# Kernel tuning notes

Measured on AMD Instinct MI355X. Metric: run time of the kernel, lower is better.

The kernel has to match this reference:

```python
import jax, jax.numpy as jnp
import numpy as np

D_IN, H, V = 512, 1024, 32000
S, B, T = 64, 128, 48
MARGIN = 0.1


def setup_inputs() -> dict:
    key = jax.random.key(0)
    ks = jax.random.split(key, 16)
    sc = 0.05
    f = lambda k, shp: jax.random.normal(k, shp, jnp.float32) * sc
    emb_W = f(ks[0], (V, D_IN)).at[0].set(0.0)  # padding_idx=0 row is zero
    return dict(
        ctx=jax.random.normal(ks[1], (S, B, H), jnp.float32),
        ctx_mask=jnp.ones((S, B), jnp.float32),
        y=jax.random.randint(ks[2], (T, B), 0, V),
        emb_W=emb_W,
        W_init=f(ks[3], (H, H)), b_init=jnp.zeros((H,), jnp.float32),
        W_ih0=f(ks[4], (3 * H, D_IN)), W_hh0=f(ks[5], (3 * H, H)),
        b_ih0=jnp.zeros((3 * H,), jnp.float32), b_hh0=jnp.zeros((3 * H,), jnp.float32),
        W_c2c=f(ks[6], (H, H)), W_h2c=f(ks[7], (H, H)), v_att=f(ks[8], (H,)),
        W_ih1=f(ks[9], (3 * H, H)), W_hh1=f(ks[10], (3 * H, H)),
        b_ih1=jnp.zeros((3 * H,), jnp.float32), b_hh1=jnp.zeros((3 * H,), jnp.float32),
        W_h2o=f(ks[11], (D_IN, H)), b_h2o=jnp.zeros((D_IN,), jnp.float32),
        W_out=f(ks[12], (V, D_IN)),
    )


def _gru(x, h, Wih, Whh, bih, bhh):
    # torch.nn.GRUCell math
    gi = x @ Wih.T + bih
    gh = h @ Whh.T + bhh
    ir, iz, inn = jnp.split(gi, 3, axis=-1)
    hr, hz, hn = jnp.split(gh, 3, axis=-1)
    r = jax.nn.sigmoid(ir + hr)
    z = jax.nn.sigmoid(iz + hz)
    n = jnp.tanh(inn + r * hn)
    return (1.0 - z) * n + z * h


def reference(ctx, ctx_mask, y, emb_W, W_init, b_init, W_ih0, W_hh0, b_ih0, b_hh0,
              W_c2c, W_h2c, v_att, W_ih1, W_hh1, b_ih1, b_hh1, W_h2o, b_h2o, W_out):
    # dec_init='mean_ctx': tanh(FF(masked mean over source))
    mean_ctx = ctx.sum(0) / ctx_mask.sum(0)[:, None]            # (B,H)
    h = jnp.tanh(mean_ctx @ W_init.T + b_init)                  # h0 (B,H)

    ctx_p = jnp.einsum('sbc,dc->sbd', ctx, W_c2c)               # ctx2ctx, hoisted out of loop
    neg = jnp.where(ctx_mask > 0, 0.0, -1e9)                    # (S,B) additive mask
    W_out_n = W_out / jnp.linalg.norm(W_out, axis=-1, keepdims=True)

    emb_in = emb_W[y[:-1]]                                      # (T-1,B,D_IN)
    targets = y[1:]                                             # (T-1,B)

    def step(h, inp):
        e, tgt = inp
        h1 = _gru(e, h, W_ih0, W_hh0, b_ih0, b_hh0)             # dec0
        # MLP attention: v^T tanh(ctx2ctx(ctx) + hid2ctx(h1))
        scores = jnp.tanh(ctx_p + (h1 @ W_h2c.T)[None]) @ v_att + neg   # (S,B)
        alpha = jax.nn.softmax(scores, axis=0)
        z_t = jnp.einsum('sb,sbc->bc', alpha, ctx)              # context (B,H)
        h2 = _gru(z_t, h1, W_ih1, W_hh1, b_ih1, b_hh1)          # dec1
        logit = jnp.tanh(h2 @ W_h2o.T + b_h2o)                  # hid2out
        logit = logit / jnp.linalg.norm(logit, axis=-1, keepdims=True)
        log_p = logit @ W_out_n.T                               # (B,V) cosine sims
        # max-margin loss, contrastive_type='max', ignore pad (tgt==0)
        s_true = jnp.take_along_axis(log_p, tgt[:, None], axis=1)
        viol = jnp.maximum(MARGIN - s_true + log_p, 0.0)
        viol = viol * (1.0 - jax.nn.one_hot(tgt, V, dtype=log_p.dtype))
        l = jnp.sum(jnp.where(tgt != 0, viol.max(-1), 0.0))
        return h2, l

    _, losses = jax.lax.scan(step, h, (emb_in, targets))
    return losses.sum()
```

## Files before the change

### kernel.cpp

```cpp
#include <hip/hip_runtime.h>
#include <math.h>

#define H    1024
#define H3   3072
#define DIN  512
#define VSZ  32000
#define SS   64
#define BB   128
#define TP   47
#define NROWS (TP*BB)
#define VCHUNKS 250
#define FMARGIN 0.1f
#define NBLK 256
#define HS   65536
#define CTXPL_S 62

typedef unsigned short u16;
typedef unsigned int u32;
typedef unsigned long long u64;
typedef __bf16 bf16_t;
typedef bf16_t bf16x8 __attribute__((ext_vector_type(8)));
typedef float f32x4 __attribute__((ext_vector_type(4)));
typedef u16 u16x4 __attribute__((ext_vector_type(4)));
typedef u16 u16x8 __attribute__((ext_vector_type(8)));

#define MFMA __builtin_amdgcn_mfma_f32_16x16x32_bf16

__device__ inline u16 f2bf(float f){
    unsigned b = __float_as_uint(f);
    return (u16)((b + 0x7FFFu + ((b >> 16) & 1u)) >> 16);
}
__device__ inline float bf2f(u16 u){ return __uint_as_float(((unsigned)u) << 16); }
__device__ inline float sigm(float x){ return 1.f/(1.f + expf(-x)); }

__device__ inline void stoval(float* p, float v){ *p = v; }
__device__ inline void stoval(u16* p, float v){ *p = f2bf(v); }

__device__ inline void cstore(u32* p, u32 v){ __hip_atomic_store(p, v, __ATOMIC_RELAXED, __HIP_MEMORY_SCOPE_AGENT); }
__device__ inline void cstoref(float* p, float v){ __hip_atomic_store(p, v, __ATOMIC_RELAXED, __HIP_MEMORY_SCOPE_AGENT); }
__device__ inline void cstore64(u64* p, u64 v){ __hip_atomic_store(p, v, __ATOMIC_RELAXED, __HIP_MEMORY_SCOPE_AGENT); }
__device__ inline float cloadf(const float* p){ return __hip_atomic_load(p, __ATOMIC_RELAXED, __HIP_MEMORY_SCOPE_AGENT); }

__device__ inline void gbar(u32* bar, u32* mygen, int tid, int bid){
    __syncthreads();
    if (tid == 0){
        u32 tgt = ++(*mygen);
        __builtin_amdgcn_s_waitcnt(0);
        u32* cnt = bar + 64 + (bid >> 3)*32;
        u32 old = __hip_atomic_fetch_add(cnt, 1u, __ATOMIC_RELAXED, __HIP_MEMORY_SCOPE_AGENT);
        if (old == 7u){
            __hip_atomic_store(cnt, 0u, __ATOMIC_RELAXED, __HIP_MEMORY_SCOPE_AGENT);
            u32 old2 = __hip_atomic_fetch_add(&bar[1], 1u, __ATOMIC_RELEASE, __HIP_MEMORY_SCOPE_AGENT);
            if (old2 == 31u){
                __hip_atomic_store(&bar[1], 0u, __ATOMIC_RELAXED, __HIP_MEMORY_SCOPE_AGENT);
                #pragma unroll
                for (int x = 0; x < 8; x++)
                    __hip_atomic_store(&bar[1536 + x*32], tgt, __ATOMIC_RELEASE, __HIP_MEMORY_SCOPE_AGENT);
            }
        }
        u32* rel = &bar[1536 + (bid & 7)*32];
        while (__hip_atomic_load(rel, __ATOMIC_RELAXED, __HIP_MEMORY_SCOPE_AGENT) < tgt)
            __builtin_amdgcn_s_sleep(2);
    }
    __syncthreads();
    asm volatile("" ::: "memory");
}


__global__ __launch_bounds__(128) void k_mask_sum(const float* __restrict__ mask, float* __restrict__ msum){
    int b = threadIdx.x;
    if (b < BB){ float s = 0.f; for (int i = 0; i < SS; i++) s += mask[i*BB + b]; msum[b] = s; }
}

__global__ __launch_bounds__(256) void k_mean_ctx(const float* __restrict__ ctx, const float* __restrict__ msum,
                                                  float* __restrict__ mean){
    int idx = blockIdx.x*256 + threadIdx.x;
    if (idx < BB*H){
        float s = 0.f;
        for (int i = 0; i < SS; i++) s += ctx[(size_t)i*BB*H + idx];
        mean[idx] = s / msum[idx / H];
    }
}

__global__ __launch_bounds__(256) void k_f32bf(const float* __restrict__ in, u16* __restrict__ out, int n4){
    int i = blockIdx.x*256 + threadIdx.x;
    if (i >= n4) return;
    float4 v = ((const float4*)in)[i];
    u16x4 o = { f2bf(v.x), f2bf(v.y), f2bf(v.z), f2bf(v.w) };
    ((u16x4*)out)[i] = o;
}

__global__ __launch_bounds__(256) void k_pack_h0(const float* __restrict__ h0, u32* __restrict__ hsHI,
                                                 u32* __restrict__ hsLO){
    int i = blockIdx.x*256 + threadIdx.x;
    float v0 = h0[i*2], v1 = h0[i*2 + 1];
    u16 a = f2bf(v0), b = f2bf(v1);
    hsHI[i] = (u32)a | ((u32)b << 16);
    hsLO[i] = (u32)f2bf(v0 - bf2f(a)) | ((u32)f2bf(v1 - bf2f(b)) << 16);
}

__global__ __launch_bounds__(256) void k_f2bf_frag(const float* __restrict__ in, u16* __restrict__ out,
                                                   int RK8, int K8){
    int t = blockIdx.x*256 + threadIdx.x;
    if (t >= RK8) return;
    int r = t / K8, k8 = t - r*K8;
    const float* p = in + (size_t)r*K8*8 + k8*8;
    float4 a = *(const float4*)p;
    float4 b = *(const float4*)(p + 4);
    size_t dst = ((size_t)(r >> 4)*(K8 >> 2) + (k8 >> 2))*512 + (size_t)((r & 15) + (k8 & 3)*16)*8;
    u16x8 o;
    o[0]=f2bf(a.x); o[1]=f2bf(a.y); o[2]=f2bf(a.z); o[3]=f2bf(a.w);
    o[4]=f2bf(b.x); o[5]=f2bf(b.y); o[6]=f2bf(b.z); o[7]=f2bf(b.w);
    *(u16x8*)(out + dst) = o;
}

// ... 69 lines not shown
        #pragma unroll
        for (int j = 0; j < 4; j++){
            float v = acc[i][j];
            if (bias) v += bias[bn + tc + j];
            if (ACT == 1) v = tanhf(v);
            C[(size_t)(bm + tr + i)*N + bn + tc + j] = v;
        }
    }
}

template<int AFRAG, int ACT, typename OutT>
__global__ __launch_bounds__(256) void k_gemmf(const u16* __restrict__ A, const u16* __restrict__ B,
                                               const float* __restrict__ bias, OutT* __restrict__ C,
                                               int M, int N, int K){
    int tid = threadIdx.x, lane = tid & 63, w = tid >> 6;
    int wm = w >> 1, wn = w & 1;
    int row0 = blockIdx.y*128 + wm*64, col0 = blockIdx.x*128 + wn*64;
    int r16 = lane & 15, kg8 = (lane >> 4)*8, rg = (lane >> 4)*4;
    int K32 = K >> 5;
    f32x4 acc[4][4] = {};
    for (int k0 = 0; k0 < K32; k0++){
        bf16x8 af[4], bfv[4];
        #pragma unroll
        for (int i = 0; i < 4; i++){
            if (AFRAG) af[i] = *(const bf16x8*)(A + (((size_t)((row0 >> 4) + i)*K32 + k0) << 9) + lane*8);
            else       af[i] = *(const bf16x8*)(A + (size_t)(row0 + i*16 + r16)*K + k0*32 + kg8);
        }
        #pragma unroll
        for (int j = 0; j < 4; j++)
            bfv[j] = *(const bf16x8*)(B + (((size_t)((col0 >> 4) + j)*K32 + k0) << 9) + lane*8);
        #pragma unroll
        for (int i = 0; i < 4; i++)
            #pragma unroll
            for (int j = 0; j < 4; j++)
                acc[i][j] = MFMA(af[i], bfv[j], acc[i][j], 0, 0, 0);
    }
    #pragma unroll
    for (int i = 0; i < 4; i++){
        #pragma unroll
        for (int j = 0; j < 4; j++){
            #pragma unroll
            for (int r = 0; r < 4; r++){
                int row = row0 + i*16 + rg + r;
                int col = col0 + j*16 + r16;
                float v = acc[i][j][r];
                if (bias) v += bias[col];
                if (ACT) v = tanhf(v);
                stoval(C + (size_t)row*N + col, v);
            }
        }
    }
}

struct RJ {
    const u16 *gi0, *Whh0, *Wh2c, *Wih1, *Whh1, *ctxp;
    const float *bhh0, *bih1, *bhh1, *vatt, *mask, *ctxf;
    u32 *hsHI, *hsLO, *h1HI, *h1LO, *ztHI, *ztLO;
    float *prF;
    float *ghF;
    float *spar;
    u32 *flg;
    u16 *h2all;
    u32 *bar;
};

__global__ __launch_bounds__(512) void k_recur9(RJ a){
    __shared__ u16 wlds[49152];
    __shared__ u16 ctxpL[CTXPL_S*512];
    __shared__ float sal[SS];
    const int tid = threadIdx.x, lane = tid & 63, wv = tid >> 6;
    const int bid = blockIdx.x;
    const int r16 = lane & 15, rg = (lane >> 4)*4, kq4 = (lane >> 4)*4;
    const int ab = (bid & 7)*16 + ((bid >> 3) >> 1);
    const int ahalf = (bid >> 3) & 1;
    u32 mygen = 0;

    {
        auto cp32k = [&](const u16* gsrc, int tile, int base){
            const u32* s = (const u32*)(gsrc + (size_t)tile*16384);
            u32* d = (u32*)(wlds + base);
            #pragma unroll
            for (int i = 0; i < 16; i++) d[tid + i*512] = s[tid + i*512];
        };
        if (bid < 64){
            cp32k(a.Whh0, bid, 0); cp32k(a.Whh0, 64+bid, 16384); cp32k(a.Whh0, 128+bid, 32768);
        } else if (bid < 128){
            int jt = bid - 64;
            cp32k(a.Wih1, jt, 0); cp32k(a.Wih1, 64+jt, 16384); cp32k(a.Wih1, 128+jt, 32768);
        } else if (bid < 192){
            int wt = bid - 128;
            cp32k(a.Whh1, 3*wt, 0); cp32k(a.Whh1, 3*wt+1, 16384); cp32k(a.Whh1, 3*wt+2, 32768);
        } else {
            cp32k(a.Wh2c, bid-192, 0);
        }
        for (int i = tid; i < CTXPL_S*512/8; i += 512){
            int s = (i*8) >> 9, h = (i*8) & 511;
            *(u16x8*)(ctxpL + i*8) = *(const u16x8*)(a.ctxp + ((size_t)(s*BB + ab))*H + ahalf*512 + h);
        }
    }
    float vv[8];
    {
        float4 v0 = *(const float4*)(a.vatt + ahalf*512 + lane*8);
        float4 v1 = *(const float4*)(a.vatt + ahalf*512 + lane*8 + 4);
        vv[0]=v0.x; vv[1]=v0.y; vv[2]=v0.z; vv[3]=v0.w;
        vv[4]=v1.x; vv[5]=v1.y; vv[6]=v1.z; vv[7]=v1.w;
    }
    __syncthreads();

    for (int t = 0; t < TP; t++){
        float* prT = a.prF + (size_t)t*BB*H;
        float* spT = a.spar + (size_t)t*256*SS;

        if (bid < 64){
            const u32* AbH = a.hsHI + (size_t)t*HS + (size_t)(wv*16 + r16)*512 + kq4;
            const u32* AbL = a.hsLO + (size_t)t*HS + (size_t)(wv*16 + r16)*512 + kq4;
            f32x4 ac0 = {}, ac1 = {}, ac2 = {};
            for (int k0 = 0; k0 < 32; k0++){
                bf16x8 ah = *(const bf16x8*)(AbH + k0*16);
                bf16x8 al = *(const bf16x8*)(AbL + k0*16);
                bf16x8 b0 = *(const bf16x8*)(wlds + (k0*64 + lane)*8);
                bf16x8 b1 = *(const bf16x8*)(wlds + 16384 + (k0*64 + lane)*8);
                bf16x8 b2 = *(const bf16x8*)(wlds + 32768 + (k0*64 + lane)*8);
                ac0 = MFMA(ah, b0, ac0, 0, 0, 0); ac0 = MFMA(al, b0, ac0, 0, 0, 0);
                ac1 = MFMA(ah, b1, ac1, 0, 0, 0); ac1 = MFMA(al, b1, ac1, 0, 0, 0);
                ac2 = MFMA(ah, b2, ac2, 0, 0, 0); ac2 = MFMA(al, b2, ac2, 0, 0, 0);
            }
            const u16* gi = a.gi0 + (size_t)t*BB*H3;
            const u32* hsH = a.hsHI + (size_t)t*HS;
            const u32* hsL = a.hsLO + (size_t)t*HS;
            int sh = (r16 & 1)*16;
            #pragma unroll
            for (int r = 0; r < 4; r++){
                int b = wv*16 + rg + r, j = bid*16 + r16;
                float gr = bf2f(gi[(size_t)b*H3 + j]);
                float gz = bf2f(gi[(size_t)b*H3 + H + j]);
                float gn = bf2f(gi[(size_t)b*H3 + 2*H + j]);
                float hr = ac0[r] + a.bhh0[j];
                float hz = ac1[r] + a.bhh0[H + j];
                float hn = ac2[r] + a.bhh0[2*H + j];
                u32 uh = hsH[(size_t)b*512 + (j >> 1)];
                u32 ul = hsL[(size_t)b*512 + (j >> 1)];
                float hp = bf2f((u16)(uh >> sh)) + bf2f((u16)(ul >> sh));
                float rr = sigm(gr + hr), zz = sigm(gz + hz);
                float nn = tanhf(gn + rr*hn);
                float hv = (1.f - zz)*nn + zz*hp;
                u16 hib = f2bf(hv);
                u16 lob = f2bf(hv - bf2f(hib));
                u32 hip = (u32)__shfl_xor((int)(u32)hib, 1);
                u32 lop = (u32)__shfl_xor((int)(u32)lob, 1);
                if (!(r16 & 1)){
                    cstore(a.h1HI + (size_t)t*HS + (size_t)b*512 + (j >> 1), (u32)hib | (hip << 16));
                    cstore(a.h1LO + (size_t)t*HS + (size_t)b*512 + (j >> 1), (u32)lob | (lop << 16));
                }
            }
        }
        gbar(a.bar, &mygen, tid, bid);

        if (bid >= 128){
            const u32* AbH = a.h1HI + (size_t)t*HS + (size_t)(wv*16 + r16)*512 + kq4;
            const u32* AbL = a.h1LO + (size_t)t*HS + (size_t)(wv*16 + r16)*512 + kq4;
            if (bid < 192){
                int wt = bid - 128;
                f32x4 ac0 = {}, ac1 = {}, ac2 = {};
                for (int k0 = 0; k0 < 32; k0++){
                    bf16x8 ah = *(const bf16x8*)(AbH + k0*16);
                    bf16x8 al = *(const bf16x8*)(AbL + k0*16);
                    bf16x8 b0 = *(const bf16x8*)(wlds + (k0*64 + lane)*8);
                    bf16x8 b1 = *(const bf16x8*)(wlds + 16384 + (k0*64 + lane)*8);
                    bf16x8 b2 = *(const bf16x8*)(wlds + 32768 + (k0*64 + lane)*8);
                    ac0 = MFMA(ah, b0, ac0, 0, 0, 0); ac0 = MFMA(al, b0, ac0, 0, 0, 0);
                    ac1 = MFMA(ah, b1, ac1, 0, 0, 0); ac1 = MFMA(al, b1, ac1, 0, 0, 0);
                    ac2 = MFMA(ah, b2, ac2, 0, 0, 0); ac2 = MFMA(al, b2, ac2, 0, 0, 0);
                }
                #pragma unroll
                for (int r = 0; r < 4; r++){
                    int b = wv*16 + rg + r;
                    int c0 = wt*48 + r16;
                    float p0 = __shfl_xor(ac0[r], 1);
                    float p1 = __shfl_xor(ac1[r], 1);
                    float p2 = __shfl_xor(ac2[r], 1);
                    if (!(r16 & 1)){
                        cstore64((u64*)(a.ghF + (size_t)b*H3 + c0),
                                 (u64)__float_as_uint(ac0[r]) | ((u64)__float_as_uint(p0) << 32));
                        cstore64((u64*)(a.ghF + (size_t)b*H3 + c0 + 16),
                                 (u64)__float_as_uint(ac1[r]) | ((u64)__float_as_uint(p1) << 32));
                        cstore64((u64*)(a.ghF + (size_t)b*H3 + c0 + 32),
                                 (u64)__float_as_uint(ac2[r]) | ((u64)__float_as_uint(p2) << 32));
                    }
                }
            } else {
                f32x4 ac = {};
                for (int k0 = 0; k0 < 32; k0++){
                    bf16x8 ah = *(const bf16x8*)(AbH + k0*16);
                    bf16x8 al = *(const bf16x8*)(AbL + k0*16);
                    bf16x8 bv = *(const bf16x8*)(wlds + (k0*64 + lane)*8);
                    ac = MFMA(ah, bv, ac, 0, 0, 0); ac = MFMA(al, bv, ac, 0, 0, 0);
                }
                #pragma unroll
                for (int r = 0; r < 4; r++){
                    int b = wv*16 + rg + r;
                    int c0 = (bid - 192)*16 + r16;
                    float p0 = __shfl_xor(ac[r], 1);
                    if (!(r16 & 1))
                        cstore64((u64*)(prT + (size_t)b*H + c0),
                                 (u64)__float_as_uint(ac[r]) | ((u64)__float_as_uint(p0) << 32));
                }
            }
        }
        gbar(a.bar, &mygen, tid, bid);

        {
            float pj[8];
            {
                float4 q0 = *(const float4*)(prT + (size_t)ab*H + ahalf*512 + lane*8);
                float4 q1 = *(const float4*)(prT + (size_t)ab*H + ahalf*512 + lane*8 + 4);
                pj[0]=q0.x; pj[1]=q0.y; pj[2]=q0.z; pj[3]=q0.w;
                pj[4]=q1.x; pj[5]=q1.y; pj[6]=q1.z; pj[7]=q1.w;
            }
            #pragma unroll
            for (int q = 0; q < 8; q++){
                int s = wv*8 + q;
                u16x8 cv;
                if (s < CTXPL_S) cv = *(const u16x8*)(ctxpL + s*512 + lane*8);
                else cv = *(const u16x8*)(a.ctxp + ((size_t)(s*BB + ab))*H + ahalf*512 + lane*8);
                float acc = 0.f;
                #pragma unroll
                for (int e = 0; e < 8; e++) acc += tanhf(bf2f(cv[e]) + pj[e]) * vv[e];
                #pragma unroll
                for (int off = 32; off; off >>= 1) acc += __shfl_xor(acc, off);
                if (lane == 0) cstoref(spT + (ab*2 + ahalf)*SS + s, acc);
            }
            __syncthreads();
            if (tid == 0){
                __builtin_amdgcn_s_waitcnt(0);
                __hip_atomic_store(&a.flg[(ab*2 + ahalf)*32], (u32)(t+1), __ATOMIC_RELEASE, __HIP_MEMORY_SCOPE_AGENT);
                while (__hip_atomic_load(&a.flg[(ab*2 + (1-ahalf))*32], __ATOMIC_ACQUIRE, __HIP_MEMORY_SCOPE_AGENT) < (u32)(t+1))
                    __builtin_amdgcn_s_sleep(1);
            }
            __syncthreads();
            if (tid < 64){
                float v = cloadf(spT + (ab*2)*SS + tid) + cloadf(spT + (ab*2 + 1)*SS + tid)
                        + ((a.mask[tid*BB + ab] > 0.f) ? 0.f : -1e9f);
                float m = v;
                #pragma unroll
                for (int off = 32; off; off >>= 1) m = fmaxf(m, __shfl_xor(m, off));
                float e = expf(v - m);
                float su = e;
                #pragma unroll
                for (int off = 32; off; off >>= 1) su += __shfl_xor(su, off);
                sal[tid] = e / su;
            }
            __syncthreads();
            int col = tid;
            const float* cbase = a.ctxf + (size_t)ab*H + ahalf*512 + col;
            float z = 0.f;
            #pragma unroll 8
            for (int s = 0; s < SS; s++)
                z += sal[s] * cbase[(size_t)s*BB*H];
            float zp = __shfl_xor(z, 1);
            if (!(tid & 1)){
                int j0 = ahalf*512 + col;
                u16 z0 = f2bf(z), z1 = f2bf(zp);
                cstore(a.ztHI + (size_t)t*HS + (size_t)ab*512 + (j0 >> 1), (u32)z0 | ((u32)z1 << 16));
                cstore(a.ztLO + (size_t)t*HS + (size_t)ab*512 + (j0 >> 1),
                       (u32)f2bf(z - bf2f(z0)) | ((u32)f2bf(zp - bf2f(z1)) << 16));
            }
            __syncthreads();
        }
        gbar(a.bar, &mygen, tid, bid);

        if (bid >= 64 && bid < 128){
            int jt = bid - 64;
            const u32* AbH = a.ztHI + (size_t)t*HS + (size_t)(wv*16 + r16)*512 + kq4;
            const u32* AbL = a.ztLO + (size_t)t*HS + (size_t)(wv*16 + r16)*512 + kq4;
            f32x4 ac0 = {}, ac1 = {}, ac2 = {};
            for (int k0 = 0; k0 < 32; k0++){
                bf16x8 ah = *(const bf16x8*)(AbH + k0*16);
                bf16x8 al = *(const bf16x8*)(AbL + k0*16);
                bf16x8 b0 = *(const bf16x8*)(wlds + (k0*64 + lane)*8);
                bf16x8 b1 = *(const bf16x8*)(wlds + 16384 + (k0*64 + lane)*8);
                bf16x8 b2 = *(const bf16x8*)(wlds + 32768 + (k0*64 + lane)*8);
                ac0 = MFMA(ah, b0, ac0, 0, 0, 0); ac0 = MFMA(al, b0, ac0, 0, 0, 0);
                ac1 = MFMA(ah, b1, ac1, 0, 0, 0); ac1 = MFMA(al, b1, ac1, 0, 0, 0);
                ac2 = MFMA(ah, b2, ac2, 0, 0, 0); ac2 = MFMA(al, b2, ac2, 0, 0, 0);
            }
            const u32* h1H = a.h1HI + (size_t)t*HS;
            const u32* h1L = a.h1LO + (size_t)t*HS;
            int sh = (r16 & 1)*16;
            #pragma unroll
            for (int r = 0; r < 4; r++){
                int b = wv*16 + rg + r, j = jt*16 + r16;
                float gr = ac0[r] + a.bih1[j];
                float gz = ac1[r] + a.bih1[H + j];
                float gn = ac2[r] + a.bih1[2*H + j];
                float hr = cloadf(a.ghF + (size_t)b*H3 + j)       + a.bhh1[j];
                float hz = cloadf(a.ghF + (size_t)b*H3 + H + j)   + a.bhh1[H + j];
                float hn = cloadf(a.ghF + (size_t)b*H3 + 2*H + j) + a.bhh1[2*H + j];
                u32 uh = h1H[(size_t)b*512 + (j >> 1)];
                u32 ul = h1L[(size_t)b*512 + (j >> 1)];
                float h1v = bf2f((u16)(uh >> sh)) + bf2f((u16)(ul >> sh));
                float rr = sigm(gr + hr), zz = sigm(gz + hz);
                float nn = tanhf(gn + rr*hn);
                float hv = (1.f - zz)*nn + zz*h1v;
                a.h2all[((size_t)t*BB + b)*H + j] = f2bf(hv);
                u16 hib = f2bf(hv);
                u16 lob = f2bf(hv - bf2f(hib));
                u32 hip = (u32)__shfl_xor((int)(u32)hib, 1);
                u32 lop = (u32)__shfl_xor((int)(u32)lob, 1);
                if (!(r16 & 1)){
                    cstore(a.hsHI + (size_t)(t+1)*HS + (size_t)b*512 + (j >> 1), (u32)hib | (hip << 16));
                    cstore(a.hsLO + (size_t)(t+1)*HS + (size_t)b*512 + (j >> 1), (u32)lob | (lop << 16));
                }
            }
        }
        gbar(a.bar, &mygen, tid, bid);
    }
}

__global__ __launch_bounds__(256) void k_final(const u16* __restrict__ logitf, const u16* __restrict__ Wf,
                                               const int* __restrict__ y, float* __restrict__ pmax,
                                               float* __restrict__ strue){
    __shared__ float red[128][2];
    int tid = threadIdx.x, w = tid >> 6, lane = tid & 63;
    int wm = w >> 1, wn = w & 1;
    int row0 = blockIdx.x*128 + wm*64;
    int col0 = blockIdx.y*128 + wn*64;
    int r16 = lane & 15, rg = (lane >> 4)*4;
    f32x4 acc[4][4] = {};
    for (int k0 = 0; k0 < 16; k0++){
        bf16x8 af[4], bfv[4];
        #pragma unroll
        for (int i = 0; i < 4; i++)
            af[i] = *(const bf16x8*)(logitf + (((size_t)((row0 >> 4) + i)*16 + k0) << 9) + lane*8);
        #pragma unroll
        for (int j = 0; j < 4; j++)
            bfv[j] = *(const bf16x8*)(Wf + (((size_t)((col0 >> 4) + j)*16 + k0) << 9) + lane*8);
        #pragma unroll
        for (int i = 0; i < 4; i++)
            #pragma unroll
            for (int j = 0; j < 4; j++)
                acc[i][j] = MFMA(af[i], bfv[j], acc[i][j], 0, 0, 0);
    }
    #pragma unroll
    for (int i = 0; i < 4; i++){
        #pragma unroll
        for (int r = 0; r < 4; r++){
            int row = row0 + i*16 + rg + r;
            int tgt = y[row + BB];
            float m = -1e30f;
            #pragma unroll
            for (int j = 0; j < 4; j++){
                float v = acc[i][j][r];
                int col = col0 + j*16 + r16;
                if (col == tgt){ strue[row] = v; v = -1e30f; }
                m = fmaxf(m, v);
            }
            m = fmaxf(m, __shfl_xor(m, 1));
            m = fmaxf(m, __shfl_xor(m, 2));
            m = fmaxf(m, __shfl_xor(m, 4));
            m = fmaxf(m, __shfl_xor(m, 8));
            if (r16 == 0) red[wm*64 + i*16 + rg + r][wn] = m;
        }
    }
    __syncthreads();
    if (tid < 128){
        float m = fmaxf(red[tid][0], red[tid][1]);
        pmax[(size_t)(blockIdx.x*128 + tid)*VCHUNKS + blockIdx.y] = m;
    }
// ... 62 lines not shown
    u16* Wh2of = (u16*)alloc((size_t)DIN*H*2);
    u16* Woutf = (u16*)alloc((size_t)VSZ*DIN*2);
    u16* ctxb  = (u16*)alloc((size_t)SS*BB*H*2);
    u16* ctxpb = (u16*)alloc((size_t)SS*BB*H*2);
    u16* embf  = (u16*)alloc((size_t)NROWS*DIN*2);
    u16* gi0b  = (u16*)alloc((size_t)NROWS*H3*2);
    u16* h2allb= (u16*)alloc((size_t)NROWS*H*2);
    u32* hsHI  = (u32*)alloc((size_t)(TP+1)*HS*4);
    u32* hsLO  = (u32*)alloc((size_t)(TP+1)*HS*4);
    u32* h1HI  = (u32*)alloc((size_t)TP*HS*4);
    u32* h1LO  = (u32*)alloc((size_t)TP*HS*4);
    u32* ztHI  = (u32*)alloc((size_t)TP*HS*4);
    u32* ztLO  = (u32*)alloc((size_t)TP*HS*4);
    float* ghF = (float*)alloc((size_t)BB*H3*4);
    float* spar= (float*)alloc((size_t)TP*256*SS*4);
    u32* bar   = (u32*)alloc(8192);
    u32* flg   = (u32*)alloc(32768);
    float* strue  = (float*)alloc(NROWS*4);
    float* msum   = (float*)alloc(BB*4);
    float* meanc  = (float*)alloc((size_t)BB*H*4);
    float* h0f    = (float*)alloc((size_t)BB*H*4);

    float* prF = (float*)Woutf;

    float* logitf  = (float*)gi0b;
    u16*   logitfr = (u16*)(gi0b + (size_t)NROWS*DIN*2);
    float* pmax    = (float*)(gi0b + (size_t)NROWS*DIN*2 + (size_t)NROWS*DIN);

    hipMemsetAsync(d_out, 0, sizeof(float), stream);
    hipMemsetAsync(bar, 0, 8192, stream);
    hipMemsetAsync(flg, 0, 32768, stream);

    hipLaunchKernelGGL(k_mask_sum, dim3(1), dim3(128), 0, stream, mask, msum);
    hipLaunchKernelGGL(k_mean_ctx, dim3(BB*H/256), dim3(256), 0, stream, ctx, msum, meanc);
    hipLaunchKernelGGL((k_gemm_nt<1>), dim3(H/64, BB/64), dim3(256), 0, stream,
                       meanc, W_init, b_init, h0f, BB, H, H);
    hipLaunchKernelGGL(k_pack_h0, dim3(HS/256), dim3(256), 0, stream, h0f, hsHI, hsLO);

    hipLaunchKernelGGL(k_f2bf_frag, dim3(H3*DIN/8/256), dim3(256), 0, stream, W_ih0, Wih0f, H3*DIN/8, DIN/8);
    hipLaunchKernelGGL(k_f2bf_frag, dim3(H3*H/8/256), dim3(256), 0, stream, W_hh0, Whh0f, H3*H/8, H/8);
    hipLaunchKernelGGL(k_f2bf_frag, dim3(H3*H/8/256), dim3(256), 0, stream, W_ih1, Wih1f, H3*H/8, H/8);
    hipLaunchKernelGGL(k_f2bf_frag, dim3(H3*H/8/256), dim3(256), 0, stream, W_hh1, Whh1f, H3*H/8, H/8);
    hipLaunchKernelGGL(k_f2bf_frag, dim3(H*H/8/256), dim3(256), 0, stream, W_h2c, Wh2cf, H*H/8, H/8);
    hipLaunchKernelGGL(k_f2bf_frag, dim3(H*H/8/256), dim3(256), 0, stream, W_c2c, Wc2cf, H*H/8, H/8);
    hipLaunchKernelGGL(k_f2bf_frag, dim3(DIN*H/8/256), dim3(256), 0, stream, W_h2o, Wh2of, DIN*H/8, H/8);
    hipLaunchKernelGGL(k_f32bf, dim3(SS*BB*H/4/256), dim3(256), 0, stream, ctx, ctxb, SS*BB*H/4);
    hipLaunchKernelGGL(k_emb_frag, dim3(NROWS/4), dim3(256), 0, stream, emb_W, y, embf);

    hipLaunchKernelGGL((k_gemmf<1,0,u16>), dim3(H3/128, NROWS/128), dim3(256), 0, stream,
                       embf, Wih0f, b_ih0, gi0b, NROWS, H3, DIN);
    hipLaunchKernelGGL((k_gemmf<0,0,u16>), dim3(H/128, SS*BB/128), dim3(256), 0, stream,
                       ctxb, Wc2cf, (const float*)nullptr, ctxpb, SS*BB, H, H);

    RJ rj;
    rj.gi0 = gi0b; rj.Whh0 = Whh0f; rj.Wh2c = Wh2cf; rj.Wih1 = Wih1f; rj.Whh1 = Whh1f;
    rj.ctxp = ctxpb;
    rj.bhh0 = b_hh0; rj.bih1 = b_ih1; rj.bhh1 = b_hh1; rj.vatt = v_att; rj.mask = mask; rj.ctxf = ctx;
    rj.hsHI = hsHI; rj.hsLO = hsLO; rj.h1HI = h1HI; rj.h1LO = h1LO; rj.ztHI = ztHI; rj.ztLO = ztLO;
    rj.prF = prF; rj.ghF = ghF; rj.spar = spar; rj.flg = flg;
    rj.h2all = h2allb; rj.bar = bar;
    void* kp[] = { (void*)&rj };
    hipLaunchCooperativeKernel((const void*)k_recur9, dim3(NBLK), dim3(512), kp, 0, stream);

    hipLaunchKernelGGL(k_rownorm_frag, dim3(VSZ/4), dim3(256), 0, stream, W_out, Woutf, VSZ);
    hipLaunchKernelGGL((k_gemmf<0,1,float>), dim3(DIN/128, NROWS/128), dim3(256), 0, stream,
                       h2allb, Wh2of, b_h2o, logitf, NROWS, DIN, H);
    hipLaunchKernelGGL(k_rownorm_frag, dim3(NROWS/4), dim3(256), 0, stream, logitf, logitfr, NROWS);
    hipLaunchKernelGGL(k_final, dim3(NROWS/128, VSZ/128), dim3(256), 0, stream,
                       logitfr, Woutf, y, pmax, strue);
    hipLaunchKernelGGL(k_loss, dim3((NROWS + 255)/256), dim3(256), 0, stream, pmax, strue, y, out);
}
```

Measured before the change: 4.785 ms.

## Replace grid-wide barriers in recurrent kernel with role-specific dataflow counters

The persistent recurrent kernel no longer runs four grid-wide barriers per timestep. Each block role (dec0 GRU, Wih1 GEMM, Whh1 GEMM, hid2ctx projection) now increments and waits on monotonic per-stage counters, so each role waits only for the data it depends on. This lets the Whh1 hidden GEMM overlap with the attention phase and cuts barrier round-trip latency on the serial critical path. In exchange it depends on correct counter targets, zeroed counters at launch, and careful ordering to avoid write-after-read hazards on single-buffered ghF.

```diff
diff --git a/kernel.cpp b/kernel.cpp
--- a/kernel.cpp
+++ b/kernel.cpp
@@ -41,26 +41,17 @@
 __device__ inline void cstore64(u64* p, u64 v){ __hip_atomic_store(p, v, __ATOMIC_RELAXED, __HIP_MEMORY_SCOPE_AGENT); }
 __device__ inline float cloadf(const float* p){ return __hip_atomic_load(p, __ATOMIC_RELAXED, __HIP_MEMORY_SCOPE_AGENT); }
 
-__device__ inline void gbar(u32* bar, u32* mygen, int tid, int bid){
+__device__ inline void cprod(u32* c, int tid){
     __syncthreads();
     if (tid == 0){
-        u32 tgt = ++(*mygen);
         __builtin_amdgcn_s_waitcnt(0);
-        u32* cnt = bar + 64 + (bid >> 3)*32;
-        u32 old = __hip_atomic_fetch_add(cnt, 1u, __ATOMIC_RELAXED, __HIP_MEMORY_SCOPE_AGENT);
-        if (old == 7u){
-            __hip_atomic_store(cnt, 0u, __ATOMIC_RELAXED, __HIP_MEMORY_SCOPE_AGENT);
-            u32 old2 = __hip_atomic_fetch_add(&bar[1], 1u, __ATOMIC_RELEASE, __HIP_MEMORY_SCOPE_AGENT);
-            if (old2 == 31u){
-                __hip_atomic_store(&bar[1], 0u, __ATOMIC_RELAXED, __HIP_MEMORY_SCOPE_AGENT);
-                #pragma unroll
-                for (int x = 0; x < 8; x++)
-                    __hip_atomic_store(&bar[1536 + x*32], tgt, __ATOMIC_RELEASE, __HIP_MEMORY_SCOPE_AGENT);
-            }
-        }
-        u32* rel = &bar[1536 + (bid & 7)*32];
-        while (__hip_atomic_load(rel, __ATOMIC_RELAXED, __HIP_MEMORY_SCOPE_AGENT) < tgt)
-            __builtin_amdgcn_s_sleep(2);
+        __hip_atomic_fetch_add(c, 1u, __ATOMIC_RELEASE, __HIP_MEMORY_SCOPE_AGENT);
+    }
+}
+__device__ inline void cwait(u32* c, u32 tgt, int tid){
+    if (tid == 0){
+        while (__hip_atomic_load(c, __ATOMIC_ACQUIRE, __HIP_MEMORY_SCOPE_AGENT) < tgt)
+            __builtin_amdgcn_s_sleep(1);
     }
     __syncthreads();
     asm volatile("" ::: "memory");
@@ -236,7 +227,7 @@
     }
 }
 
-struct RJ {
+struct RK {
     const u16 *gi0, *Whh0, *Wh2c, *Wih1, *Whh1, *ctxp;
     const float *bhh0, *bih1, *bhh1, *vatt, *mask, *ctxf;
     u32 *hsHI, *hsLO, *h1HI, *h1LO, *ztHI, *ztLO;
@@ -248,7 +239,7 @@
     u32 *bar;
 };
 
-__global__ __launch_bounds__(512) void k_recur9(RJ a){
+__global__ __launch_bounds__(512) void k_recur10(RK a){
     __shared__ u16 wlds[49152];
     __shared__ u16 ctxpL[CTXPL_S*512];
     __shared__ float sal[SS];
@@ -257,7 +248,10 @@
     const int r16 = lane & 15, rg = (lane >> 4)*4, kq4 = (lane >> 4)*4;
     const int ab = (bid & 7)*16 + ((bid >> 3) >> 1);
     const int ahalf = (bid >> 3) & 1;
-    u32 mygen = 0;
+    u32* sA = a.bar + 0;
+    u32* sB = a.bar + 32;
+    u32* sC = a.bar + 64;
+    u32* sD = a.bar + 96;
 
     {
         auto cp32k = [&](const u16* gsrc, int tile, int base){
@@ -291,213 +285,246 @@
     }
     __syncthreads();
 
-    for (int t = 0; t < TP; t++){
+    auto P1 = [&](int t){
+        const u32* AbH = a.hsHI + (size_t)t*HS + (size_t)(wv*16 + r16)*512 + kq4;
+        const u32* AbL = a.hsLO + (size_t)t*HS + (size_t)(wv*16 + r16)*512 + kq4;
+        f32x4 ac0 = {}, ac1 = {}, ac2 = {};
+        for (int k0 = 0; k0 < 32; k0++){
+            bf16x8 ah = *(const bf16x8*)(AbH + k0*16);
+            bf16x8 al = *(const bf16x8*)(AbL + k0*16);
+            bf16x8 b0 = *(const bf16x8*)(wlds + (k0*64 + lane)*8);
+            bf16x8 b1 = *(const bf16x8*)(wlds + 16384 + (k0*64 + lane)*8);
+            bf16x8 b2 = *(const bf16x8*)(wlds + 32768 + (k0*64 + lane)*8);
+            ac0 = MFMA(ah, b0, ac0, 0, 0, 0); ac0 = MFMA(al, b0, ac0, 0, 0, 0);
+            ac1 = MFMA(ah, b1, ac1, 0, 0, 0); ac1 = MFMA(al, b1, ac1, 0, 0, 0);
+            ac2 = MFMA(ah, b2, ac2, 0, 0, 0); ac2 = MFMA(al, b2, ac2, 0, 0, 0);
+        }
+        const u16* gi = a.gi0 + (size_t)t*BB*H3;
+        const u32* hsH = a.hsHI + (size_t)t*HS;
+        const u32* hsL = a.hsLO + (size_t)t*HS;
+        int sh = (r16 & 1)*16;
+        #pragma unroll
+        for (int r = 0; r < 4; r++){
+            int b = wv*16 + rg + r, j = bid*16 + r16;
+            float gr = bf2f(gi[(size_t)b*H3 + j]);
+            float gz = bf2f(gi[(size_t)b*H3 + H + j]);
+            float gn = bf2f(gi[(size_t)b*H3 + 2*H + j]);
+            float hr = ac0[r] + a.bhh0[j];
+            float hz = ac1[r] + a.bhh0[H + j];
+            float hn = ac2[r] + a.bhh0[2*H + j];
+            u32 uh = hsH[(size_t)b*512 + (j >> 1)];
+            u32 ul = hsL[(size_t)b*512 + (j >> 1)];
+            float hp = bf2f((u16)(uh >> sh)) + bf2f((u16)(ul >> sh));
+            float rr = sigm(gr + hr), zz = sigm(gz + hz);
+            float nn = tanhf(gn + rr*hn);
+            float hv = (1.f - zz)*nn + zz*hp;
+            u16 hib = f2bf(hv);
+            u16 lob = f2bf(hv - bf2f(hib));
+            u32 hip = (u32)__shfl_xor((int)(u32)hib, 1);
+            u32 lop = (u32)__shfl_xor((int)(u32)lob, 1);
+            if (!(r16 & 1)){
+                cstore(a.h1HI + (size_t)t*HS + (size_t)b*512 + (j >> 1), (u32)hib | (hip << 16));
+                cstore(a.h1LO + (size_t)t*HS + (size_t)b*512 + (j >> 1), (u32)lob | (lop << 16));
+            }
+        }
+    };
+
+    auto P2gh1 = [&](int t){
+        const u32* AbH = a.h1HI + (size_t)t*HS + (size_t)(wv*16 + r16)*512 + kq4;
+        const u32* AbL = a.h1LO + (size_t)t*HS + (size_t)(wv*16 + r16)*512 + kq4;
+        int wt = bid - 128;
+        f32x4 ac0 = {}, ac1 = {}, ac2 = {};
+        for (int k0 = 0; k0 < 32; k0++){
+            bf16x8 ah = *(const bf16x8*)(AbH + k0*16);
+            bf16x8 al = *(const bf16x8*)(AbL + k0*16);
+            bf16x8 b0 = *(const bf16x8*)(wlds + (k0*64 + lane)*8);
+            bf16x8 b1 = *(const bf16x8*)(wlds + 16384 + (k0*64 + lane)*8);
+            bf16x8 b2 = *(const bf16x8*)(wlds + 32768 + (k0*64 + lane)*8);
+            ac0 = MFMA(ah, b0, ac0, 0, 0, 0); ac0 = MFMA(al, b0, ac0, 0, 0, 0);
+            ac1 = MFMA(ah, b1, ac1, 0, 0, 0); ac1 = MFMA(al, b1, ac1, 0, 0, 0);
+            ac2 = MFMA(ah, b2, ac2, 0, 0, 0); ac2 = MFMA(al, b2, ac2, 0, 0, 0);
+        }
+        #pragma unroll
+        for (int r = 0; r < 4; r++){
+            int b = wv*16 + rg + r;
+            int c0 = wt*48 + r16;
+            float p0 = __shfl_xor(ac0[r], 1);
+            float p1 = __shfl_xor(ac1[r], 1);
+            float p2 = __shfl_xor(ac2[r], 1);
+            if (!(r16 & 1)){
+                cstore64((u64*)(a.ghF + (size_t)b*H3 + c0),
+                         (u64)__float_as_uint(ac0[r]) | ((u64)__float_as_uint(p0) << 32));
+                cstore64((u64*)(a.ghF + (size_t)b*H3 + c0 + 16),
+                         (u64)__float_as_uint(ac1[r]) | ((u64)__float_as_uint(p1) << 32));
+                cstore64((u64*)(a.ghF + (size_t)b*H3 + c0 + 32),
+                         (u64)__float_as_uint(ac2[r]) | ((u64)__float_as_uint(p2) << 32));
+            }
+        }
+    };
+
+    auto P2proj = [&](int t){
+        float* prT = a.prF + (size_t)t*BB*H;
+        const u32* AbH = a.h1HI + (size_t)t*HS + (size_t)(wv*16 + r16)*512 + kq4;
+        const u32* AbL = a.h1LO + (size_t)t*HS + (size_t)(wv*16 + r16)*512 + kq4;
+        f32x4 ac = {};
+        for (int k0 = 0; k0 < 32; k0++){
+            bf16x8 ah = *(const bf16x8*)(AbH + k0*16);
+            bf16x8 al = *(const bf16x8*)(AbL + k0*16);
+            bf16x8 bv = *(const bf16x8*)(wlds + (k0*64 + lane)*8);
+            ac = MFMA(ah, bv, ac, 0, 0, 0); ac = MFMA(al, bv, ac, 0, 0, 0);
+        }
+        #pragma unroll
+        for (int r = 0; r < 4; r++){
+            int b = wv*16 + rg + r;
+            int c0 = (bid - 192)*16 + r16;
+            float p0 = __shfl_xor(ac[r], 1);
+            if (!(r16 & 1))
+                cstore64((u64*)(prT + (size_t)b*H + c0),
+                         (u64)__float_as_uint(ac[r]) | ((u64)__float_as_uint(p0) << 32));
+        }
+    };
+
+    auto P3 = [&](int t){
         float* prT = a.prF + (size_t)t*BB*H;
         float* spT = a.spar + (size_t)t*256*SS;
-
-        if (bid < 64){
-            const u32* AbH = a.hsHI + (size_t)t*HS + (size_t)(wv*16 + r16)*512 + kq4;
-            const u32* AbL = a.hsLO + (size_t)t*HS + (size_t)(wv*16 + r16)*512 + kq4;
-            f32x4 ac0 = {}, ac1 = {}, ac2 = {};
-            for (int k0 = 0; k0 < 32; k0++){
-                bf16x8 ah = *(const bf16x8*)(AbH + k0*16);
-                bf16x8 al = *(const bf16x8*)(AbL + k0*16);
-                bf16x8 b0 = *(const bf16x8*)(wlds + (k0*64 + lane)*8);
-                bf16x8 b1 = *(const bf16x8*)(wlds + 16384 + (k0*64 + lane)*8);
-                bf16x8 b2 = *(const bf16x8*)(wlds + 32768 + (k0*64 + lane)*8);
-                ac0 = MFMA(ah, b0, ac0, 0, 0, 0); ac0 = MFMA(al, b0, ac0, 0, 0, 0);
-                ac1 = MFMA(ah, b1, ac1, 0, 0, 0); ac1 = MFMA(al, b1, ac1, 0, 0, 0);
-                ac2 = MFMA(ah, b2, ac2, 0, 0, 0); ac2 = MFMA(al, b2, ac2, 0, 0, 0);
+        float pj[8];
+        {
+            float4 q0 = *(const float4*)(prT + (size_t)ab*H + ahalf*512 + lane*8);
+            float4 q1 = *(const float4*)(prT + (size_t)ab*H + ahalf*512 + lane*8 + 4);
+            pj[0]=q0.x; pj[1]=q0.y; pj[2]=q0.z; pj[3]=q0.w;
+            pj[4]=q1.x; pj[5]=q1.y; pj[6]=q1.z; pj[7]=q1.w;
+        }
+        #pragma unroll
+        for (int q = 0; q < 8; q++){
+            int s = wv*8 + q;
+            u16x8 cv;
+            if (s < CTXPL_S) cv = *(const u16x8*)(ctxpL + s*512 + lane*8);
+            else cv = *(const u16x8*)(a.ctxp + ((size_t)(s*BB + ab))*H + ahalf*512 + lane*8);
+            float acc = 0.f;
+            #pragma unroll
+            for (int e = 0; e < 8; e++) acc += tanhf(bf2f(cv[e]) + pj[e]) * vv[e];
+            #pragma unroll
+            for (int off = 32; off; off >>= 1) acc += __shfl_xor(acc, off);
+            if (lane == 0) cstoref(spT + (ab*2 + ahalf)*SS + s, acc);
+        }
+        __syncthreads();
+        if (tid == 0){
+            __builtin_amdgcn_s_waitcnt(0);
+            __hip_atomic_store(&a.flg[(ab*2 + ahalf)*32], (u32)(t+1), __ATOMIC_RELEASE, __HIP_MEMORY_SCOPE_AGENT);
+            while (__hip_atomic_load(&a.flg[(ab*2 + (1-ahalf))*32], __ATOMIC_ACQUIRE, __HIP_MEMORY_SCOPE_AGENT) < (u32)(t+1))
+                __builtin_amdgcn_s_sleep(1);
+        }
+        __syncthreads();
+        if (tid < 64){
+            float v = cloadf(spT + (ab*2)*SS + tid) + cloadf(spT + (ab*2 + 1)*SS + tid)
+                    + ((a.mask[tid*BB + ab] > 0.f) ? 0.f : -1e9f);
+            float m = v;
+            #pragma unroll
+            for (int off = 32; off; off >>= 1) m = fmaxf(m, __shfl_xor(m, off));
+            float e = expf(v - m);
+            float su = e;
+            #pragma unroll
+            for (int off = 32; off; off >>= 1) su += __shfl_xor(su, off);
+            sal[tid] = e / su;
+        }
+        __syncthreads();
+        int col = tid;
+        const float* cbase = a.ctxf + (size_t)ab*H + ahalf*512 + col;
+        float z = 0.f;
+        #pragma unroll 8
+        for (int s = 0; s < SS; s++)
+            z += sal[s] * cbase[(size_t)s*BB*H];
+        float zp = __shfl_xor(z, 1);
+        if (!(tid & 1)){
+            int j0 = ahalf*512 + col;
+            u16 z0 = f2bf(z), z1 = f2bf(zp);
+            cstore(a.ztHI + (size_t)t*HS + (size_t)ab*512 + (j0 >> 1), (u32)z0 | ((u32)z1 << 16));
+            cstore(a.ztLO + (size_t)t*HS + (size_t)ab*512 + (j0 >> 1),
+                   (u32)f2bf(z - bf2f(z0)) | ((u32)f2bf(zp - bf2f(z1)) << 16));
+        }
+        __syncthreads();
+    };
+
+    auto P4 = [&](int t){
+        int jt = bid - 64;
+        const u32* AbH = a.ztHI + (size_t)t*HS + (size_t)(wv*16 + r16)*512 + kq4;
+        const u32* AbL = a.ztLO + (size_t)t*HS + (size_t)(wv*16 + r16)*512 + kq4;
+        f32x4 ac0 = {}, ac1 = {}, ac2 = {};
+        for (int k0 = 0; k0 < 32; k0++){
+            bf16x8 ah = *(const bf16x8*)(AbH + k0*16);
+            bf16x8 al = *(const bf16x8*)(AbL + k0*16);
+            bf16x8 b0 = *(const bf16x8*)(wlds + (k0*64 + lane)*8);
+            bf16x8 b1 = *(const bf16x8*)(wlds + 16384 + (k0*64 + lane)*8);
+            bf16x8 b2 = *(const bf16x8*)(wlds + 32768 + (k0*64 + lane)*8);
+            ac0 = MFMA(ah, b0, ac0, 0, 0, 0); ac0 = MFMA(al, b0, ac0, 0, 0, 0);
+            ac1 = MFMA(ah, b1, ac1, 0, 0, 0); ac1 = MFMA(al, b1, ac1, 0, 0, 0);
+            ac2 = MFMA(ah, b2, ac2, 0, 0, 0); ac2 = MFMA(al, b2, ac2, 0, 0, 0);
+        }
+        const u32* h1H = a.h1HI + (size_t)t*HS;
+        const u32* h1L = a.h1LO + (size_t)t*HS;
+        int sh = (r16 & 1)*16;
+        #pragma unroll
+        for (int r = 0; r < 4; r++){
+            int b = wv*16 + rg + r, j = jt*16 + r16;
+            float gr = ac0[r] + a.bih1[j];
+            float gz = ac1[r] + a.bih1[H + j];
+            float gn = ac2[r] + a.bih1[2*H + j];
+            float hr = cloadf(a.ghF + (size_t)b*H3 + j)       + a.bhh1[j];
+            float hz = cloadf(a.ghF + (size_t)b*H3 + H + j)   + a.bhh1[H + j];
+            float hn = cloadf(a.ghF + (size_t)b*H3 + 2*H + j) + a.bhh1[2*H + j];
+            u32 uh = h1H[(size_t)b*512 + (j >> 1)];
+            u32 ul = h1L[(size_t)b*512 + (j >> 1)];
+            float h1v = bf2f((u16)(uh >> sh)) + bf2f((u16)(ul >> sh));
+            float rr = sigm(gr + hr), zz = sigm(gz + hz);
+            float nn = tanhf(gn + rr*hn);
+            float hv = (1.f - zz)*nn + zz*h1v;
+            a.h2all[((size_t)t*BB + b)*H + j] = f2bf(hv);
+            u16 hib = f2bf(hv);
+            u16 lob = f2bf(hv - bf2f(hib));
+            u32 hip = (u32)__shfl_xor((int)(u32)hib, 1);
+            u32 lop = (u32)__shfl_xor((int)(u32)lob, 1);
+            if (!(r16 & 1)){
+                cstore(a.hsHI + (size_t)(t+1)*HS + (size_t)b*512 + (j >> 1), (u32)hib | (hip << 16));
+                cstore(a.hsLO + (size_t)(t+1)*HS + (size_t)b*512 + (j >> 1), (u32)lob | (lop << 16));
             }
-            const u16* gi = a.gi0 + (size_t)t*BB*H3;
-            const u32* hsH = a.hsHI + (size_t)t*HS;
-            const u32* hsL = a.hsLO + (size_t)t*HS;
-            int sh = (r16 & 1)*16;
-            #pragma unroll
-            for (int r = 0; r < 4; r++){
-                int b = wv*16 + rg + r, j = bid*16 + r16;
-                float gr = bf2f(gi[(size_t)b*H3 + j]);
-                float gz = bf2f(gi[(size_t)b*H3 + H + j]);
-                float gn = bf2f(gi[(size_t)b*H3 + 2*H + j]);
-                float hr = ac0[r] + a.bhh0[j];
-                float hz = ac1[r] + a.bhh0[H + j];
-                float hn = ac2[r] + a.bhh0[2*H + j];
-                u32 uh = hsH[(size_t)b*512 + (j >> 1)];
-                u32 ul = hsL[(size_t)b*512 + (j >> 1)];
-                float hp = bf2f((u16)(uh >> sh)) + bf2f((u16)(ul >> sh));
-                float rr = sigm(gr + hr), zz = sigm(gz + hz);
-                float nn = tanhf(gn + rr*hn);
-                float hv = (1.f - zz)*nn + zz*hp;
-                u16 hib = f2bf(hv);
-                u16 lob = f2bf(hv - bf2f(hib));
-                u32 hip = (u32)__shfl_xor((int)(u32)hib, 1);
-                u32 lop = (u32)__shfl_xor((int)(u32)lob, 1);
-                if (!(r16 & 1)){
-                    cstore(a.h1HI + (size_t)t*HS + (size_t)b*512 + (j >> 1), (u32)hib | (hip << 16));
-                    cstore(a.h1LO + (size_t)t*HS + (size_t)b*512 + (j >> 1), (u32)lob | (lop << 16));
-                }
-            }
-        }
-        gbar(a.bar, &mygen, tid, bid);
-
-        if (bid >= 128){
-            const u32* AbH = a.h1HI + (size_t)t*HS + (size_t)(wv*16 + r16)*512 + kq4;
-            const u32* AbL = a.h1LO + (size_t)t*HS + (size_t)(wv*16 + r16)*512 + kq4;
-            if (bid < 192){
-                int wt = bid - 128;
-                f32x4 ac0 = {}, ac1 = {}, ac2 = {};
-                for (int k0 = 0; k0 < 32; k0++){
-                    bf16x8 ah = *(const bf16x8*)(AbH + k0*16);
-                    bf16x8 al = *(const bf16x8*)(AbL + k0*16);
-                    bf16x8 b0 = *(const bf16x8*)(wlds + (k0*64 + lane)*8);
-                    bf16x8 b1 = *(const bf16x8*)(wlds + 16384 + (k0*64 + lane)*8);
-                    bf16x8 b2 = *(const bf16x8*)(wlds + 32768 + (k0*64 + lane)*8);
-                    ac0 = MFMA(ah, b0, ac0, 0, 0, 0); ac0 = MFMA(al, b0, ac0, 0, 0, 0);
-                    ac1 = MFMA(ah, b1, ac1, 0, 0, 0); ac1 = MFMA(al, b1, ac1, 0, 0, 0);
-                    ac2 = MFMA(ah, b2, ac2, 0, 0, 0); ac2 = MFMA(al, b2, ac2, 0, 0, 0);
-                }
-                #pragma unroll
-                for (int r = 0; r < 4; r++){
-                    int b = wv*16 + rg + r;
-                    int c0 = wt*48 + r16;
-                    float p0 = __shfl_xor(ac0[r], 1);
-                    float p1 = __shfl_xor(ac1[r], 1);
-                    float p2 = __shfl_xor(ac2[r], 1);
-                    if (!(r16 & 1)){
-                        cstore64((u64*)(a.ghF + (size_t)b*H3 + c0),
-                                 (u64)__float_as_uint(ac0[r]) | ((u64)__float_as_uint(p0) << 32));
-                        cstore64((u64*)(a.ghF + (size_t)b*H3 + c0 + 16),
-                                 (u64)__float_as_uint(ac1[r]) | ((u64)__float_as_uint(p1) << 32));
-                        cstore64((u64*)(a.ghF + (size_t)b*H3 + c0 + 32),
-                                 (u64)__float_as_uint(ac2[r]) | ((u64)__float_as_uint(p2) << 32));
-                    }
-                }
-            } else {
-                f32x4 ac = {};
-                for (int k0 = 0; k0 < 32; k0++){
-                    bf16x8 ah = *(const bf16x8*)(AbH + k0*16);
-                    bf16x8 al = *(const bf16x8*)(AbL + k0*16);
-                    bf16x8 bv = *(const bf16x8*)(wlds + (k0*64 + lane)*8);
-                    ac = MFMA(ah, bv, ac, 0, 0, 0); ac = MFMA(al, bv, ac, 0, 0, 0);
-                }
-                #pragma unroll
-                for (int r = 0; r < 4; r++){
-                    int b = wv*16 + rg + r;
-                    int c0 = (bid - 192)*16 + r16;
-                    float p0 = __shfl_xor(ac[r], 1);
-                    if (!(r16 & 1))
-                        cstore64((u64*)(prT + (size_t)b*H + c0),
-                                 (u64)__float_as_uint(ac[r]) | ((u64)__float_as_uint(p0) << 32));
-                }
-            }
-        }
-        gbar(a.bar, &mygen, tid, bid);
-
-        {
-            float pj[8];
-            {
-                float4 q0 = *(const float4*)(prT + (size_t)ab*H + ahalf*512 + lane*8);
-                float4 q1 = *(const float4*)(prT + (size_t)ab*H + ahalf*512 + lane*8 + 4);
-                pj[0]=q0.x; pj[1]=q0.y; pj[2]=q0.z; pj[3]=q0.w;
-                pj[4]=q1.x; pj[5]=q1.y; pj[6]=q1.z; pj[7]=q1.w;
-            }
-            #pragma unroll
-            for (int q = 0; q < 8; q++){
-                int s = wv*8 + q;
-                u16x8 cv;
-                if (s < CTXPL_S) cv = *(const u16x8*)(ctxpL + s*512 + lane*8);
-                else cv = *(const u16x8*)(a.ctxp + ((size_t)(s*BB + ab))*H + ahalf*512 + lane*8);
-                float acc = 0.f;
-                #pragma unroll
-                for (int e = 0; e < 8; e++) acc += tanhf(bf2f(cv[e]) + pj[e]) * vv[e];
-                #pragma unroll
-                for (int off = 32; off; off >>= 1) acc += __shfl_xor(acc, off);
-                if (lane == 0) cstoref(spT + (ab*2 + ahalf)*SS + s, acc);
-            }
-            __syncthreads();
-            if (tid == 0){
-                __builtin_amdgcn_s_waitcnt(0);
-                __hip_atomic_store(&a.flg[(ab*2 + ahalf)*32], (u32)(t+1), __ATOMIC_RELEASE, __HIP_MEMORY_SCOPE_AGENT);
-                while (__hip_atomic_load(&a.flg[(ab*2 + (1-ahalf))*32], __ATOMIC_ACQUIRE, __HIP_MEMORY_SCOPE_AGENT) < (u32)(t+1))
-                    __builtin_amdgcn_s_sleep(1);
-            }
-            __syncthreads();
-            if (tid < 64){
-                float v = cloadf(spT + (ab*2)*SS + tid) + cloadf(spT + (ab*2 + 1)*SS + tid)
-                        + ((a.mask[tid*BB + ab] > 0.f) ? 0.f : -1e9f);
-                float m = v;
-                #pragma unroll
-                for (int off = 32; off; off >>= 1) m = fmaxf(m, __shfl_xor(m, off));
-                float e = expf(v - m);
-                float su = e;
-                #pragma unroll
-                for (int off = 32; off; off >>= 1) su += __shfl_xor(su, off);
-                sal[tid] = e / su;
-            }
-            __syncthreads();
-            int col = tid;
-            const float* cbase = a.ctxf + (size_t)ab*H + ahalf*512 + col;
-            float z = 0.f;
-            #pragma unroll 8
-            for (int s = 0; s < SS; s++)
-                z += sal[s] * cbase[(size_t)s*BB*H];
-            float zp = __shfl_xor(z, 1);
-            if (!(tid & 1)){
-                int j0 = ahalf*512 + col;
-                u16 z0 = f2bf(z), z1 = f2bf(zp);
-                cstore(a.ztHI + (size_t)t*HS + (size_t)ab*512 + (j0 >> 1), (u32)z0 | ((u32)z1 << 16));
-                cstore(a.ztLO + (size_t)t*HS + (size_t)ab*512 + (j0 >> 1),
-                       (u32)f2bf(z - bf2f(z0)) | ((u32)f2bf(zp - bf2f(z1)) << 16));
-            }
-            __syncthreads();
-        }
-        gbar(a.bar, &mygen, tid, bid);
-
-        if (bid >= 64 && bid < 128){
-            int jt = bid - 64;
-            const u32* AbH = a.ztHI + (size_t)t*HS + (size_t)(wv*16 + r16)*512 + kq4;
-            const u32* AbL = a.ztLO + (size_t)t*HS + (size_t)(wv*16 + r16)*512 + kq4;
-            f32x4 ac0 = {}, ac1 = {}, ac2 = {};
-            for (int k0 = 0; k0 < 32; k0++){
-                bf16x8 ah = *(const bf16x8*)(AbH + k0*16);
-                bf16x8 al = *(const bf16x8*)(AbL + k0*16);
-                bf16x8 b0 = *(const bf16x8*)(wlds + (k0*64 + lane)*8);
-                bf16x8 b1 = *(const bf16x8*)(wlds + 16384 + (k0*64 + lane)*8);
-                bf16x8 b2 = *(const bf16x8*)(wlds + 32768 + (k0*64 + lane)*8);
-                ac0 = MFMA(ah, b0, ac0, 0, 0, 0); ac0 = MFMA(al, b0, ac0, 0, 0, 0);
-                ac1 = MFMA(ah, b1, ac1, 0, 0, 0); ac1 = MFMA(al, b1, ac1, 0, 0, 0);
-                ac2 = MFMA(ah, b2, ac2, 0, 0, 0); ac2 = MFMA(al, b2, ac2, 0, 0, 0);
-            }
-            const u32* h1H = a.h1HI + (size_t)t*HS;
-            const u32* h1L = a.h1LO + (size_t)t*HS;
-            int sh = (r16 & 1)*16;
-            #pragma unroll
-            for (int r = 0; r < 4; r++){
-                int b = wv*16 + rg + r, j = jt*16 + r16;
-                float gr = ac0[r] + a.bih1[j];
-                float gz = ac1[r] + a.bih1[H + j];
-                float gn = ac2[r] + a.bih1[2*H + j];
-                float hr = cloadf(a.ghF + (size_t)b*H3 + j)       + a.bhh1[j];
-                float hz = cloadf(a.ghF + (size_t)b*H3 + H + j)   + a.bhh1[H + j];
-                float hn = cloadf(a.ghF + (size_t)b*H3 + 2*H + j) + a.bhh1[2*H + j];
-                u32 uh = h1H[(size_t)b*512 + (j >> 1)];
-                u32 ul = h1L[(size_t)b*512 + (j >> 1)];
-                float h1v = bf2f((u16)(uh >> sh)) + bf2f((u16)(ul >> sh));
-                float rr = sigm(gr + hr), zz = sigm(gz + hz);
-                float nn = tanhf(gn + rr*hn);
-                float hv = (1.f - zz)*nn + zz*h1v;
-                a.h2all[((size_t)t*BB + b)*H + j] = f2bf(hv);
-                u16 hib = f2bf(hv);
-                u16 lob = f2bf(hv - bf2f(hib));
-                u32 hip = (u32)__shfl_xor((int)(u32)hib, 1);
-                u32 lop = (u32)__shfl_xor((int)(u32)lob, 1);
-                if (!(r16 & 1)){
-                    cstore(a.hsHI + (size_t)(t+1)*HS + (size_t)b*512 + (j >> 1), (u32)hib | (hip << 16));
-                    cstore(a.hsLO + (size_t)(t+1)*HS + (size_t)b*512 + (j >> 1), (u32)lob | (lop << 16));
-                }
-            }
-        }
-        gbar(a.bar, &mygen, tid, bid);
+        }
+    };
+
+    if (bid < 64){
+        for (int t = 0; t < TP; t++){
+            cwait(sD, 64u*t, tid);
+            P1(t);
+            cprod(sA, tid);
+            cwait(sB, 64u*(t+1), tid);
+            P3(t);
+            cprod(sC, tid);
+        }
+    } else if (bid < 128){
+        for (int t = 0; t < TP; t++){
+            cwait(sB, 64u*(t+1), tid);
+            P3(t);
+            cprod(sC, tid);
+            cwait(sC, 256u*(t+1), tid);
+            P4(t);
+            cprod(sD, tid);
+        }
+    } else if (bid < 192){
+        for (int t = 0; t < TP; t++){
+            cwait(sA, 64u*(t+1), tid);
+            P2gh1(t);
+            cwait(sB, 64u*(t+1), tid);
+            P3(t);
+            cprod(sC, tid);
+        }
+    } else {
+        for (int t = 0; t < TP; t++){
+            cwait(sA, 64u*(t+1), tid);
+            P2proj(t);
+            cprod(sB, tid);
+            cwait(sB, 64u*(t+1), tid);
+            P3(t);
+            cprod(sC, tid);
+        }
     }
 }
 
@@ -666,15 +693,15 @@
     hipLaunchKernelGGL((k_gemmf<0,0,u16>), dim3(H/128, SS*BB/128), dim3(256), 0, stream,
                        ctxb, Wc2cf, (const float*)nullptr, ctxpb, SS*BB, H, H);
 
-    RJ rj;
-    rj.gi0 = gi0b; rj.Whh0 = Whh0f; rj.Wh2c = Wh2cf; rj.Wih1 = Wih1f; rj.Whh1 = Whh1f;
-    rj.ctxp = ctxpb;
-    rj.bhh0 = b_hh0; rj.bih1 = b_ih1; rj.bhh1 = b_hh1; rj.vatt = v_att; rj.mask = mask; rj.ctxf = ctx;
-    rj.hsHI = hsHI; rj.hsLO = hsLO; rj.h1HI = h1HI; rj.h1LO = h1LO; rj.ztHI = ztHI; rj.ztLO = ztLO;
-    rj.prF = prF; rj.ghF = ghF; rj.spar = spar; rj.flg = flg;
-    rj.h2all = h2allb; rj.bar = bar;
-    void* kp[] = { (void*)&rj };
-    hipLaunchCooperativeKernel((const void*)k_recur9, dim3(NBLK), dim3(512), kp, 0, stream);
+    RK rk;
+    rk.gi0 = gi0b; rk.Whh0 = Whh0f; rk.Wh2c = Wh2cf; rk.Wih1 = Wih1f; rk.Whh1 = Whh1f;
+    rk.ctxp = ctxpb;
+    rk.bhh0 = b_hh0; rk.bih1 = b_ih1; rk.bhh1 = b_hh1; rk.vatt = v_att; rk.mask = mask; rk.ctxf = ctx;
+    rk.hsHI = hsHI; rk.hsLO = hsLO; rk.h1HI = h1HI; rk.h1LO = h1LO; rk.ztHI = ztHI; rk.ztLO = ztLO;
+    rk.prF = prF; rk.ghF = ghF; rk.spar = spar; rk.flg = flg;
+    rk.h2all = h2allb; rk.bar = bar;
+    void* kp[] = { (void*)&rk };
+    hipLaunchCooperativeKernel((const void*)k_recur10, dim3(NBLK), dim3(512), kp, 0, stream);
 
     hipLaunchKernelGGL(k_rownorm_frag, dim3(VSZ/4), dim3(256), 0, stream, W_out, Woutf, VSZ);
     hipLaunchKernelGGL((k_gemmf<0,1,float>), dim3(DIN/128, NROWS/128), dim3(256), 0, stream,
```

Measured after the change: 12.64 ms. +164.2%, slower.
